# Optimization experiments

Measured on AMD Instinct MI355X. Metric: run time of the kernel, lower is better.

## Reference

```python
import jax, jax.numpy as jnp
import numpy as np

B, S = 1, 2048
D = 4096          # hidden_size
H, HK, DH = 32, 8, 128  # num_heads, num_kv_heads, head_dim
THETA = 10000.0


def setup_inputs() -> dict:
    key = jax.random.key(0)
    k0, k1, k2, k3, k4 = jax.random.split(key, 5)
    std = 0.02
    return {
        "position_ids": jnp.broadcast_to(jnp.arange(S, dtype=jnp.int32), (B, S)),
        "hidden_states": jax.random.normal(k0, (B, S, D), jnp.float32),
        "Wq": (jax.random.normal(k1, (D, H * DH), jnp.float32) * std),
        "Wk": (jax.random.normal(k2, (D, HK * DH), jnp.float32) * std),
        "Wv": (jax.random.normal(k3, (D, HK * DH), jnp.float32) * std),
        "Wo": (jax.random.normal(k4, (H * DH, D), jnp.float32) * std),
    }


def _rope(x, pos):
    """Neox-style rotary embedding over the full head_dim. x: [B,S,h,DH]."""
    half = DH // 2
    inv_freq = 1.0 / (THETA ** (jnp.arange(half, dtype=jnp.float32) * 2.0 / DH))
    ang = pos[..., None].astype(jnp.float32) * inv_freq          # [B,S,half]
    cos = jnp.cos(ang)[:, :, None, :]
    sin = jnp.sin(ang)[:, :, None, :]
    x1, x2 = x[..., :half], x[..., half:]
    return jnp.concatenate([x1 * cos - x2 * sin, x2 * cos + x1 * sin], axis=-1)


def reference(position_ids, hidden_states, Wq, Wk, Wv, Wo):
    q = (hidden_states @ Wq).reshape(B, S, H, DH)
    k = (hidden_states @ Wk).reshape(B, S, HK, DH)
    v = (hidden_states @ Wv).reshape(B, S, HK, DH)
    q = _rope(q, position_ids)
    k = _rope(k, position_ids)

    G = H // HK  # query heads per kv head (GQA)
    qg = q.reshape(B, S, HK, G, DH)
    scale = jnp.float32(DH) ** -0.5
    scores = jnp.einsum('bqhgd,bkhd->bhgqk', qg, k) * scale      # [B,HK,G,S,S]
    causal = jnp.tril(jnp.ones((S, S), dtype=bool))
    scores = jnp.where(causal, scores, jnp.finfo(scores.dtype).min)
    p = jax.nn.softmax(scores, axis=-1)
    out = jnp.einsum('bhgqk,bkhd->bqhgd', p, v).reshape(B, S, H * DH)
    return out @ Wo
```

## Files before the change

### kernel.cpp

```cpp
#include <hip/hip_runtime.h>

typedef unsigned short u16;
typedef short bf16x8 __attribute__((ext_vector_type(8)));
typedef float f32x4 __attribute__((ext_vector_type(4)));

#define GLB __attribute__((address_space(1)))
#define LDSAS __attribute__((address_space(3)))

constexpr int S = 2048, D = 4096, NH = 32, NHK = 8, DHD = 128;
constexpr int NQKV = 6144;

__device__ __forceinline__ u16 f2b(float f) {
    union { float f; unsigned u; } v; v.f = f;
    return (u16)((v.u + 0x7fffu + ((v.u >> 16) & 1u)) >> 16);
}
__device__ __forceinline__ float b2f(u16 b) {
    union { unsigned u; float f; } v; v.u = ((unsigned)b) << 16;
    return v.f;
}
__device__ __forceinline__ void gload16(const void* g, void* l) {
    __builtin_amdgcn_global_load_lds((const GLB unsigned int*)g,
                                     (LDSAS unsigned int*)l, 16, 0, 0);
}
#if __has_builtin(__builtin_amdgcn_exp2f)
__device__ __forceinline__ float exp2fast(float x) { return __builtin_amdgcn_exp2f(x); }
#else
__device__ __forceinline__ float exp2fast(float x) { return __expf(0.6931471805599453f * x); }
#endif

__device__ __forceinline__ void sincos_big(float ang, float* sn, float* cs) {
#if __has_builtin(__builtin_amdgcn_sinf) && __has_builtin(__builtin_amdgcn_cosf)
    float rev = ang * 0.15915494309189535f;
    rev = rev - floorf(rev);
    *sn = __builtin_amdgcn_sinf(rev);
    *cs = __builtin_amdgcn_cosf(rev);
#else
    *sn = sinf(ang);
    *cs = cosf(ang);
#endif
}

__global__ __launch_bounds__(256) void cvt_x(const float* __restrict__ in,
                                             u16* __restrict__ out, int n8) {
    int i = blockIdx.x * 256 + threadIdx.x;
    if (i >= n8) return;
    const float4* p = (const float4*)in + (size_t)i * 2;
    float4 a = p[0], b = p[1];
    uint4 o;
    o.x = f2b(a.x) | ((unsigned)f2b(a.y) << 16);
    o.y = f2b(a.z) | ((unsigned)f2b(a.w) << 16);
    o.z = f2b(b.x) | ((unsigned)f2b(b.y) << 16);
    o.w = f2b(b.z) | ((unsigned)f2b(b.w) << 16);
    *(uint4*)(out + (size_t)i * 8) = o;
}

__global__ __launch_bounds__(256) void tconvV(const float* __restrict__ in,
                                              u16* __restrict__ out, int R, int C) {
    __shared__ float t[64][65];
    const int r0 = blockIdx.y * 64, c0 = blockIdx.x * 64;
    const int tid = threadIdx.x;
    const int rr = tid >> 4;
    const int cc = (tid & 15) * 4;
#pragma unroll
    for (int p = 0; p < 4; ++p) {
        int r = p * 16 + rr;
        float4 v = *(const float4*)&in[(size_t)(r0 + r) * C + c0 + cc];
        t[r][cc] = v.x; t[r][cc + 1] = v.y; t[r][cc + 2] = v.z; t[r][cc + 3] = v.w;
    }
    __syncthreads();
#pragma unroll
    for (int p = 0; p < 4; ++p) {
        int c = p * 16 + rr;
        ushort4 o;
        o.x = f2b(t[cc + 0][c]); o.y = f2b(t[cc + 1][c]);
        o.z = f2b(t[cc + 2][c]); o.w = f2b(t[cc + 3][c]);
        *(ushort4*)&out[(size_t)(c0 + c) * R + r0 + cc] = o;
    }
}

__global__ __launch_bounds__(256) void vtransV(const u16* __restrict__ QKV,
                                               u16* __restrict__ Vt) {
    __shared__ u16 t[64][65];
    const int hk = blockIdx.z;
    const int s0 = blockIdx.x * 64, d0 = blockIdx.y * 64;
    const int tid = threadIdx.x;
    const int rr = tid >> 4;
    const int cc = (tid & 15) * 4;
#pragma unroll
    for (int p = 0; p < 4; ++p) {
        int s = p * 16 + rr;
        ushort4 v = *(const ushort4*)&QKV[(size_t)(s0 + s) * NQKV + 5120 + hk * 128 + d0 + cc];
        t[s][cc] = v.x; t[s][cc + 1] = v.y; t[s][cc + 2] = v.z; t[s][cc + 3] = v.w;
    }
    __syncthreads();
#pragma unroll
    for (int p = 0; p < 4; ++p) {
        int d = p * 16 + rr;
        ushort4 o;
        o.x = t[cc + 0][d]; o.y = t[cc + 1][d];
        o.z = t[cc + 2][d]; o.w = t[cc + 3][d];
        *(ushort4*)&Vt[(size_t)hk * (128 * 2048) + (size_t)(d0 + d) * 2048 + s0 + cc] = o;
    }
}

__global__ __launch_bounds__(256) void ropeM(u16* __restrict__ T,
                                             const int* __restrict__ pos, float sc2) {
    const int hh = blockIdx.y;
    const int i = blockIdx.x * 256 + threadIdx.x;
    const int d = i & 63;
    const int s = i >> 6;
    const float scale = hh < 32 ? sc2 : 1.0f;
    float p = (float)pos[s];
    float inv = __expf(-(float)d * 0.14391156531310576f);
    float ang = p * inv;
    float sn, cs;
    sincos_big(ang, &sn, &cs);
    size_t base = (size_t)s * NQKV + hh * 128 + d;
    float x1 = b2f(T[base]), x2 = b2f(T[base + 64]);
    T[base]      = f2b((x1 * cs - x2 * sn) * scale);
    T[base + 64] = f2b((x2 * cs + x1 * sn) * scale);
}

template <bool BF16OUT>
__global__ __launch_bounds__(256) void gemmS(const u16* __restrict__ A,
                                             const u16* __restrict__ Bt,
                                             void* __restrict__ Cout,
                                             int N, int K, int nbx) {
    __shared__ u16 Asm[128 * 64];
    __shared__ u16 Bsm[128 * 64];
    const int xcd = (int)blockIdx.x & 7;
    const int slot = (int)blockIdx.x >> 3;
    const int nby = (int)gridDim.x / nbx;
    const int rpb = nby >> 1;
    const int cpb = nbx >> 2;
    const int by = (xcd >> 2) * rpb + slot / cpb;
    const int bx = (xcd & 3) * cpb + slot % cpb;
    const int m0 = by * 128, n0 = bx * 128;
    const int tid = threadIdx.x, lane = tid & 63, wave = tid >> 6;
    const int l15 = lane & 15, l4 = lane >> 4;
    const int wm = wave >> 1, wn = wave & 1;
    f32x4 acc[4][4] = {};

    for (int k0 = 0; k0 < K; k0 += 64) {
        __syncthreads();
#pragma unroll
        for (int u = 0; u < 4; ++u) {
            int s = u * 256 + tid;
            int row = s >> 3, cs = (s & 7) ^ (row & 7);
            gload16(A  + (size_t)(m0 + row) * K + k0 + cs * 8, Asm + s * 8);
            gload16(Bt + (size_t)(n0 + row) * K + k0 + cs * 8, Bsm + s * 8);
        }
        __syncthreads();
        bf16x8 af[4][2], bf[4][2];
#pragma unroll
        for (int i = 0; i < 4; ++i)
#pragma unroll
            for (int kk = 0; kk < 2; ++kk) {
                int row = wm * 64 + i * 16 + l15;
                int cc = (kk * 4 + l4) ^ (row & 7);
                af[i][kk] = *(const bf16x8*)(Asm + row * 64 + cc * 8);
            }
#pragma unroll
        for (int j = 0; j < 4; ++j)
#pragma unroll
            for (int kk = 0; kk < 2; ++kk) {
                int row = wn * 64 + j * 16 + l15;
                int cc = (kk * 4 + l4) ^ (row & 7);
                bf[j][kk] = *(const bf16x8*)(Bsm + row * 64 + cc * 8);
            }
#pragma unroll
        for (int i = 0; i < 4; ++i)
#pragma unroll
            for (int j = 0; j < 4; ++j)
#pragma unroll
                for (int kk = 0; kk < 2; ++kk)
                    acc[i][j] = __builtin_amdgcn_mfma_f32_16x16x32_bf16(af[i][kk], bf[j][kk], acc[i][j], 0, 0, 0);
    }
#pragma unroll
    for (int i = 0; i < 4; ++i)
#pragma unroll
        for (int j = 0; j < 4; ++j) {
            int col  = n0 + wn * 64 + j * 16 + l15;
            int rowb = m0 + wm * 64 + i * 16 + l4 * 4;
#pragma unroll
            for (int r = 0; r < 4; ++r) {
                if (BF16OUT)
                    ((u16*)Cout)[(size_t)(rowb + r) * N + col] = f2b(acc[i][j][r]);
                else
                    ((float*)Cout)[(size_t)(rowb + r) * N + col] = acc[i][j][r];
            }
        }
}

__global__ __launch_bounds__(256) void attn3(const u16* __restrict__ QKV,
                                             const u16* __restrict__ Vt,
                                             u16* __restrict__ O) {
    __shared__ u16 Ksm[2][64 * 128];
    __shared__ u16 Vsm[2][128 * 64];
    __shared__ u16 Psm[4][16 * 64];
    const int orig = blockIdx.x;
    const int swz = (orig & 7) * 64 + (orig >> 3);
    const int h = swz >> 4, p = swz & 15;
    const int hk = h >> 2;
    const int tid = threadIdx.x, wave = tid >> 6, lane = tid & 63;
    const int l15 = lane & 15, l4 = lane >> 4;
    const u16* Qp = QKV + h * 128;
    const u16* Kp = QKV + 4096 + hk * 128;
    const u16* Vp = Vt + (size_t)hk * (128 * 2048);

    auto stage = [&](int kb, int b) {
#pragma unroll
        for (int it = 0; it < 4; ++it) {
            int L = it * 256 + tid;
            int krow = L >> 4, kslot = L & 15;
            int kcs = (kslot & 8) | ((kslot ^ krow) & 7);
            gload16(Kp + (size_t)(kb * 64 + krow) * NQKV + kcs * 8, &Ksm[b][L * 8]);
            int vrow = L >> 3, vslot = L & 7;
            int vcs = (vslot ^ vrow) & 7;
            gload16(Vp + (size_t)vrow * 2048 + kb * 64 + vcs * 8, &Vsm[b][L * 8]);
        }
    };

#pragma unroll 1
    for (int pass = 0; pass < 2; ++pass) {
        const int qt = pass ? p : 31 - p;
        const int qr0 = qt * 64 + wave * 16;
        const int nkb = qt + 1;

        bf16x8 qf[4];
        {
            const u16* qrow = Qp + (size_t)(qr0 + l15) * NQKV;
#pragma unroll
            for (int c = 0; c < 4; ++c)
                qf[c] = *(const bf16x8*)(qrow + c * 32 + l4 * 8);
        }
        float mrow[4], lsum[4];
#pragma unroll
        for (int r = 0; r < 4; ++r) { mrow[r] = -1e30f; lsum[r] = 0.f; }
        f32x4 o[8] = {};

        stage(0, 0);
#pragma unroll 1
        for (int kb = 0; kb < nkb; ++kb) {
            const int cur = kb & 1;
            if (kb + 1 < nkb) {
                stage(kb + 1, cur ^ 1);
                asm volatile("s_waitcnt vmcnt(8)" ::: "memory");
            } else {
                asm volatile("s_waitcnt vmcnt(0)" ::: "memory");
            }
            __builtin_amdgcn_s_barrier();

            if (kb * 64 <= qr0 + 15) {
                const u16* Kb_ = Ksm[cur];
                const u16* Vb_ = Vsm[cur];
                const bool diag = (kb * 64 + 63 > qr0);
                f32x4 sc[4] = {};
#pragma unroll
                for (int f = 0; f < 4; ++f) {
                    const int kv = f * 16 + l15;
#pragma unroll
                    for (int c = 0; c < 4; ++c) {
                        int cd = c * 4 + l4;
                        int cpos = (cd & 8) | ((cd ^ kv) & 7);
                        bf16x8 kf = *(const bf16x8*)(Kb_ + kv * 128 + cpos * 8);
                        sc[f] = __builtin_amdgcn_mfma_f32_16x16x32_bf16(qf[c], kf, sc[f], 0, 0, 0);
                    }
                }
                if (diag) {
#pragma unroll
                    for (int f = 0; f < 4; ++f) {
                        int col = kb * 64 + f * 16 + l15;
#pragma unroll
                        for (int r = 0; r < 4; ++r) {
                            int row = qr0 + l4 * 4 + r;
                            if (col > row) sc[f][r] = -1e30f;
                        }
                    }
                }
                float bm[4];
#pragma unroll
                for (int r = 0; r < 4; ++r)
                    bm[r] = fmaxf(fmaxf(sc[0][r], sc[1][r]), fmaxf(sc[2][r], sc[3][r]));
                bool need = false;
#pragma unroll
                for (int r = 0; r < 4; ++r) need = need || (bm[r] > mrow[r] + 8.0f);
                if (__any((int)need)) {
#pragma unroll
                    for (int msk = 1; msk < 16; msk <<= 1)
#pragma unroll
                        for (int r = 0; r < 4; ++r) bm[r] = fmaxf(bm[r], __shfl_xor(bm[r], msk));
                    float al[4];
#pragma unroll
                    for (int r = 0; r < 4; ++r) {
                        float mn = fmaxf(mrow[r], bm[r]);
                        al[r] = exp2fast(mrow[r] - mn);
                        mrow[r] = mn;
                        lsum[r] *= al[r];
                    }
#pragma unroll
                    for (int n = 0; n < 8; ++n)
#pragma unroll
                        for (int r = 0; r < 4; ++r) o[n][r] *= al[r];
                }
#pragma unroll
                for (int f = 0; f < 4; ++f) {
#pragma unroll
                    for (int r = 0; r < 4; ++r) {
                        float pw = exp2fast(sc[f][r] - mrow[r]);
                        lsum[r] += pw;
                        int q = l4 * 4 + r;
                        int kvc = f * 2 + (l15 >> 3);
                        int slot = (kvc ^ q) & 7;
                        Psm[wave][q * 64 + slot * 8 + (l15 & 7)] = f2b(pw);
                    }
                }

                asm volatile("s_waitcnt lgkmcnt(0)" ::: "memory");
                bf16x8 pf[2];
#pragma unroll
                for (int c = 0; c < 2; ++c) {
                    int chc = c * 4 + l4;
                    int slot = (chc ^ l15) & 7;
                    pf[c] = *(const bf16x8*)(&Psm[wave][l15 * 64 + slot * 8]);
                }
#pragma unroll
                for (int n = 0; n < 8; ++n) {
                    int d = n * 16 + l15;
                    bf16x8 vf[2];
#pragma unroll
                    for (int c = 0; c < 2; ++c) {
                        int ch = c * 4 + l4;
                        int slot = (ch ^ d) & 7;
                        vf[c] = *(const bf16x8*)(Vb_ + d * 64 + slot * 8);
                    }
#pragma unroll
                    for (int c = 0; c < 2; ++c)
                        o[n] = __builtin_amdgcn_mfma_f32_16x16x32_bf16(pf[c], vf[c], o[n], 0, 0, 0);
                }
            }
            asm volatile("s_waitcnt lgkmcnt(0)" ::: "memory");
            __builtin_amdgcn_s_barrier();
        }

#pragma unroll
        for (int msk = 1; msk < 16; msk <<= 1)
#pragma unroll
            for (int r = 0; r < 4; ++r) lsum[r] += __shfl_xor(lsum[r], msk);
        float inv[4];
#pragma unroll
        for (int r = 0; r < 4; ++r) inv[r] = 1.0f / lsum[r];
#pragma unroll
        for (int n = 0; n < 8; ++n)
#pragma unroll
            for (int r = 0; r < 4; ++r) {
                int row = qr0 + l4 * 4 + r;
                O[(size_t)row * 4096 + h * 128 + n * 16 + l15] = f2b(o[n][r] * inv[r]);
            }
    }
}

extern "C" void kernel_launch(void* const* d_in, const int* in_sizes, int n_in,
                              void* d_out, int out_size, void* d_ws, size_t ws_size,
                              hipStream_t stream) {
    const int*   pos = (const int*)d_in[0];
    const float* X   = (const float*)d_in[1];
    const float* Wq  = (const float*)d_in[2];
    const float* Wk  = (const float*)d_in[3];
    const float* Wv  = (const float*)d_in[4];
    const float* Wo  = (const float*)d_in[5];
    float* out = (float*)d_out;

    char* w = (char*)d_ws;
    u16* Xb    = (u16*)(w + 0);
    u16* Wqkvt = (u16*)(w + 16777216);
    u16* Wot   = (u16*)(w + 67108864);
    u16* QKV   = (u16*)(w + 100663296);
    u16* Vtb   = (u16*)(w + 125829120);
    u16* Ob    = (u16*)(w + 130023424);

    const float SC2 = 0.08838834764831845f * 1.4426950408889634f;

    cvt_x<<<4096, 256, 0, stream>>>(X, Xb, S * D / 8);
    tconvV<<<dim3(64, 64), 256, 0, stream>>>(Wq, Wqkvt, 4096, 4096);
    tconvV<<<dim3(16, 64), 256, 0, stream>>>(Wk, Wqkvt + (size_t)4096 * 4096, 4096, 1024);
    tconvV<<<dim3(16, 64), 256, 0, stream>>>(Wv, Wqkvt + (size_t)5120 * 4096, 4096, 1024);
    tconvV<<<dim3(64, 64), 256, 0, stream>>>(Wo, Wot, 4096, 4096);

    gemmS<true><<<768, 256, 0, stream>>>(Xb, Wqkvt, QKV, NQKV, 4096, 48);

    ropeM<<<dim3(512, 40), 256, 0, stream>>>(QKV, pos, SC2);

    vtransV<<<dim3(32, 2, 8), 256, 0, stream>>>(QKV, Vtb);

    attn3<<<512, 256, 0, stream>>>(QKV, Vtb, Ob);

    gemmS<false><<<512, 256, 0, stream>>>(Ob, Wot, out, 4096, 4096, 32);
}
```

Measured before the change: 344.7 us.

## Split-K the output projection GEMM into two halves with bf16 partials and reduce

The output projection GEMM is now split along K into two chunks, doubling the grid to 1024 blocks so the 256-CU GPU gets more than one wave of work. Each chunk writes a bf16 partial into reused workspace, and a new reduction kernel sums the two partials into the fp32 output. This trades better occupancy and load balance for an extra kernel launch, extra partial-buffer traffic, and extra precision loss from rounding partials to bf16.

```diff
diff --git a/kernel.cpp b/kernel.cpp
--- a/kernel.cpp
+++ b/kernel.cpp
@@ -52,6 +52,25 @@
     o.z = f2b(b.x) | ((unsigned)f2b(b.y) << 16);
     o.w = f2b(b.z) | ((unsigned)f2b(b.w) << 16);
     *(uint4*)(out + (size_t)i * 8) = o;
+}
+
+__global__ __launch_bounds__(256) void red2(const u16* __restrict__ P,
+                                            float* __restrict__ out, int n8) {
+    int i = blockIdx.x * 256 + threadIdx.x;
+    if (i >= n8) return;
+    uint4 a = *(const uint4*)(P + (size_t)i * 8);
+    uint4 b = *(const uint4*)(P + (size_t)8388608 + (size_t)i * 8);
+    float4 o0, o1;
+    o0.x = b2f((u16)a.x) + b2f((u16)b.x);
+    o0.y = b2f((u16)(a.x >> 16)) + b2f((u16)(b.x >> 16));
+    o0.z = b2f((u16)a.y) + b2f((u16)b.y);
+    o0.w = b2f((u16)(a.y >> 16)) + b2f((u16)(b.y >> 16));
+    o1.x = b2f((u16)a.z) + b2f((u16)b.z);
+    o1.y = b2f((u16)(a.z >> 16)) + b2f((u16)(b.z >> 16));
+    o1.z = b2f((u16)a.w) + b2f((u16)b.w);
+    o1.w = b2f((u16)(a.w >> 16)) + b2f((u16)(b.w >> 16));
+    float4* q = (float4*)(out + (size_t)i * 8);
+    q[0] = o0; q[1] = o1;
 }
 
 __global__ __launch_bounds__(256) void tconvV(const float* __restrict__ in,
@@ -125,30 +144,36 @@
 __global__ __launch_bounds__(256) void gemmS(const u16* __restrict__ A,
                                              const u16* __restrict__ Bt,
                                              void* __restrict__ Cout,
-                                             int N, int K, int nbx) {
+                                             int N, int Kstride, int nbx,
+                                             int kch, int klen) {
     __shared__ u16 Asm[128 * 64];
     __shared__ u16 Bsm[128 * 64];
     const int xcd = (int)blockIdx.x & 7;
-    const int slot = (int)blockIdx.x >> 3;
-    const int nby = (int)gridDim.x / nbx;
+    const int gslot = (int)blockIdx.x >> 3;
+    const int ks = gslot % kch;
+    const int slot = gslot / kch;
+    const int nper = (int)gridDim.x / kch;
+    const int nby = nper / nbx;
     const int rpb = nby >> 1;
     const int cpb = nbx >> 2;
     const int by = (xcd >> 2) * rpb + slot / cpb;
     const int bx = (xcd & 3) * cpb + slot % cpb;
     const int m0 = by * 128, n0 = bx * 128;
+    const int kbeg = ks * klen;
+    const size_t obase = (size_t)ks * 2048 * N;
     const int tid = threadIdx.x, lane = tid & 63, wave = tid >> 6;
     const int l15 = lane & 15, l4 = lane >> 4;
     const int wm = wave >> 1, wn = wave & 1;
     f32x4 acc[4][4] = {};
 
-    for (int k0 = 0; k0 < K; k0 += 64) {
+    for (int k0 = kbeg; k0 < kbeg + klen; k0 += 64) {
         __syncthreads();
 #pragma unroll
         for (int u = 0; u < 4; ++u) {
             int s = u * 256 + tid;
             int row = s >> 3, cs = (s & 7) ^ (row & 7);
-            gload16(A  + (size_t)(m0 + row) * K + k0 + cs * 8, Asm + s * 8);
-            gload16(Bt + (size_t)(n0 + row) * K + k0 + cs * 8, Bsm + s * 8);
+            gload16(A  + (size_t)(m0 + row) * Kstride + k0 + cs * 8, Asm + s * 8);
+            gload16(Bt + (size_t)(n0 + row) * Kstride + k0 + cs * 8, Bsm + s * 8);
         }
         __syncthreads();
         bf16x8 af[4][2], bf[4][2];
@@ -185,9 +210,9 @@
 #pragma unroll
             for (int r = 0; r < 4; ++r) {
                 if (BF16OUT)
-                    ((u16*)Cout)[(size_t)(rowb + r) * N + col] = f2b(acc[i][j][r]);
+                    ((u16*)Cout)[obase + (size_t)(rowb + r) * N + col] = f2b(acc[i][j][r]);
                 else
-                    ((float*)Cout)[(size_t)(rowb + r) * N + col] = acc[i][j][r];
+                    ((float*)Cout)[obase + (size_t)(rowb + r) * N + col] = acc[i][j][r];
             }
         }
 }
@@ -378,6 +403,7 @@
     u16* QKV   = (u16*)(w + 100663296);
     u16* Vtb   = (u16*)(w + 125829120);
     u16* Ob    = (u16*)(w + 130023424);
+    u16* Pp    = (u16*)(w + 0);
 
     const float SC2 = 0.08838834764831845f * 1.4426950408889634f;
 
@@ -387,7 +413,7 @@
     tconvV<<<dim3(16, 64), 256, 0, stream>>>(Wv, Wqkvt + (size_t)5120 * 4096, 4096, 1024);
     tconvV<<<dim3(64, 64), 256, 0, stream>>>(Wo, Wot, 4096, 4096);
 
-    gemmS<true><<<768, 256, 0, stream>>>(Xb, Wqkvt, QKV, NQKV, 4096, 48);
+    gemmS<true><<<768, 256, 0, stream>>>(Xb, Wqkvt, QKV, NQKV, 4096, 48, 1, 4096);
 
     ropeM<<<dim3(512, 40), 256, 0, stream>>>(QKV, pos, SC2);
 
@@ -395,5 +421,6 @@
 
     attn3<<<512, 256, 0, stream>>>(QKV, Vtb, Ob);
 
-    gemmS<false><<<512, 256, 0, stream>>>(Ob, Wot, out, 4096, 4096, 32);
-}
+    gemmS<true><<<1024, 256, 0, stream>>>(Ob, Wot, Pp, 4096, 4096, 32, 2, 2048);
+    red2<<<4096, 256, 0, stream>>>(Pp, out, 1048576);
+}
```

Measured after the change: 365.8 us. +6.1%, slower.
